# Kernel tuning notes

Measured on AMD Instinct MI355X. Metric: run time of the kernel, lower is better.

Reference implementation:

```python
import jax, jax.numpy as jnp
import numpy as np

N, M, D = 2048, 100000, 128
K = 5


def setup_inputs() -> dict:
    key = jax.random.key(0)
    k1, k2 = jax.random.split(key)
    features = jax.random.normal(k1, (N, D), dtype=jnp.float32)
    memory_bank = jax.random.normal(k2, (M, D), dtype=jnp.float32)
    # normalization buffers computed during fit(); use plausible scalars
    min_val = jnp.zeros((), dtype=jnp.float32)
    max_val = jnp.ones((), dtype=jnp.float32)
    return {
        "features": features,
        "memory_bank": memory_bank,
        "min_val": min_val,
        "max_val": max_val,
        "n_neighbors": K,
    }


def reference(features, memory_bank, min_val, max_val, n_neighbors):
    x2 = jnp.sum(features * features, axis=1, keepdims=True)        # (N,1)
    y2 = jnp.sum(memory_bank * memory_bank, axis=1)[None, :]        # (1,M)
    d2 = x2 + y2 - 2.0 * (features @ memory_bank.T)                 # (N,M)
    dist = jnp.sqrt(jnp.maximum(d2, 0.0))
    # k smallest distances per query (topk largest=False)
    neg_knn, _ = jax.lax.top_k(-dist, n_neighbors)                  # (N,K)
    knn = -neg_knn
    # min-max normalization with fitted stats
    knn = (knn - min_val) / (max_val - min_val)
    return knn.mean(axis=1)                                         # (N,)
```

## Files before the change

### kernel.cpp

```cpp
#include <hip/hip_runtime.h>
#include <stdint.h>

#define N_Q 2048
#define M_B 100000
#define D_DIM 128
#define KNN 5
#define SLABS_TOTAL 1563
#define M_PAD (SLABS_TOTAL * 64)
#define CHUNKS 64
#define SPC 25
#define CLS 16
#define FTOT (CHUNKS * CLS)
#define ROWBLOCKS 8
#define TROWS 256
#define RT 4
#define BIGF 3.0e38f
#define NEGF -3.0e38f


typedef __attribute__((ext_vector_type(8))) short short8;
typedef __attribute__((ext_vector_type(4))) unsigned short ushort4v;
typedef __attribute__((ext_vector_type(8))) unsigned short ushort8v;
typedef __attribute__((ext_vector_type(4))) float f32x4;

static __device__ __forceinline__ unsigned short f2bf(float f) {
  unsigned int u = __builtin_bit_cast(unsigned int, f);
  u = (u + 0x7FFFu + ((u >> 16) & 1u)) >> 16;
  return (unsigned short)u;
}

static __device__ __forceinline__ void gload_lds16(const void* g, void* l) {
  __builtin_amdgcn_global_load_lds((const __attribute__((address_space(1))) unsigned int*)g,
                                   (__attribute__((address_space(3))) unsigned int*)l, 16, 0, 0);
}
static __device__ __forceinline__ void gload_lds4(const void* g, void* l) {
  __builtin_amdgcn_global_load_lds((const __attribute__((address_space(1))) unsigned int*)g,
                                   (__attribute__((address_space(3))) unsigned int*)l, 4, 0, 0);
}

#define DPPADD(v, ctrl)                                                              \
  do {                                                                               \
    int _t = __builtin_amdgcn_update_dpp(0, __builtin_bit_cast(int, (v)), (ctrl),    \
                                         0xf, 0xf, false);                           \
    (v) = (v) + __builtin_bit_cast(float, _t);                                       \
  } while (0)

__global__ __launch_bounds__(256) void k_prep(const float* __restrict__ Y,
                                              unsigned short* __restrict__ ybf,
                                              float* __restrict__ ny2) {
  const int s = blockIdx.x;
  const int t = threadIdx.x;
  __shared__ __align__(16) unsigned short tile[8192];
  __shared__ float redy[64 * 33];
#pragma unroll
  for (int i = 0; i < 8; ++i) {
    const int u = i * 256 + t;
    const int rowl = u >> 5;
    const int q = u & 31;
    const int rowg = s * 64 + rowl;
    const int rowc = (rowg < M_B) ? rowg : (M_B - 1);
    const float4 v = ((const float4*)Y)[(size_t)rowc * 32 + q];
    redy[rowl * 33 + q] = v.x * v.x + v.y * v.y + v.z * v.z + v.w * v.w;
    ushort4v o;
    o[0] = f2bf(v.x); o[1] = f2bf(v.y); o[2] = f2bf(v.z); o[3] = f2bf(v.w);
    *(ushort4v*)(tile + (size_t)(((q >> 1) * 64 + rowl) * 8 + (q & 1) * 4)) = o;
  }
  __syncthreads();
  {
    const int rowl = t >> 2;
    const int k = t & 3;
    float ss = 0.f;
#pragma unroll
    for (int j = 0; j < 8; ++j) ss += redy[rowl * 33 + k * 8 + j];
    DPPADD(ss, 0xB1);
    DPPADD(ss, 0x4E);
    const int rowg = s * 64 + rowl;
    if ((t & 3) == 0) ny2[(size_t)s * 64 + rowl] = (rowg < M_B) ? (-0.5f * ss) : NEGF;
  }
#pragma unroll
  for (int i = 0; i < 4; ++i) {
    const int u = i * 256 + t;
    *(ushort8v*)(ybf + ((size_t)s * 1024 + u) * 8) = *(const ushort8v*)(tile + u * 8);
  }
}

__global__ __launch_bounds__(256, 2) void k_main(const float* __restrict__ X,
                                                 const unsigned short* __restrict__ ybf,
                                                 const float* __restrict__ ny2,
                                                 float* __restrict__ rsm) {
  __shared__ __align__(16) char smem[39168];
  unsigned short* ys = (unsigned short*)smem;
  float* ny2s = (float*)(smem + 32768);

  const int bid = blockIdx.x;
  const int chunk = bid % CHUNKS;
  const int rowblock = bid / CHUNKS;
  const int row0 = rowblock * TROWS;

  const int cs0 = chunk * SPC;
  int nslab = SLABS_TOTAL - cs0;
  if (nslab > SPC) nslab = SPC;
  if (nslab < 0) nslab = 0;

  const int t = threadIdx.x;
  const int wave = t >> 6;
  const int lane = t & 63;
  const int lm = lane & 15;
  const int lq = lane >> 4;

  short8 afrag[RT][4];
#pragma unroll
  for (int rt = 0; rt < RT; ++rt)
#pragma unroll
    for (int ks = 0; ks < 4; ++ks) {
      const float* xr = X + (size_t)(row0 + wave * 64 + rt * 16 + lm) * D_DIM + ks * 32 + lq * 8;
      const float4 a = *(const float4*)xr;
      const float4 b = *(const float4*)(xr + 4);
      short8 f;
      f[0] = (short)f2bf(a.x); f[1] = (short)f2bf(a.y);
      f[2] = (short)f2bf(a.z); f[3] = (short)f2bf(a.w);
      f[4] = (short)f2bf(b.x); f[5] = (short)f2bf(b.y);
      f[6] = (short)f2bf(b.z); f[7] = (short)f2bf(b.w);
      afrag[rt][ks] = f;
    }

  for (int j = wave; j < nslab; j += 4)
    gload_lds4(ny2 + (size_t)(cs0 + j) * 64 + lane, ny2s + (size_t)j * 64);
  __syncthreads();

  float prmax[RT][4];
#pragma unroll
  for (int rt = 0; rt < RT; ++rt)
#pragma unroll
    for (int rr = 0; rr < 4; ++rr) prmax[rt][rr] = NEGF;

  if (nslab > 0) {
    const unsigned short* src = ybf + (size_t)cs0 * 8192;
#pragma unroll
    for (int i = 0; i < 4; ++i) {
      const int ub = i * 256 + wave * 64;
      gload_lds16(src + (size_t)(ub + lane) * 8, ys + (size_t)ub * 8);
    }
  }

  for (int s = 0; s < nslab; ++s) {
    unsigned short* yb = ys + (size_t)(s & 1) * 8192;
    if (s + 1 < nslab) {
      const unsigned short* src = ybf + (size_t)(cs0 + s + 1) * 8192;
      unsigned short* dst = ys + (size_t)((s + 1) & 1) * 8192;
#pragma unroll
      for (int i = 0; i < 4; ++i) {
        const int ub = i * 256 + wave * 64;
        gload_lds16(src + (size_t)(ub + lane) * 8, dst + (size_t)ub * 8);
      }
      asm volatile("s_waitcnt vmcnt(4)" ::: "memory");
    } else {
      asm volatile("s_waitcnt vmcnt(0)" ::: "memory");
    }
    __builtin_amdgcn_s_barrier();

    float y2c[4];
#pragma unroll
    for (int ct = 0; ct < 4; ++ct) y2c[ct] = ny2s[s * 64 + ct * 16 + lm];

    f32x4 acc[RT][4];
#pragma unroll
    for (int rt = 0; rt < RT; ++rt)
#pragma unroll
      for (int ct = 0; ct < 4; ++ct)
#pragma unroll
        for (int rr = 0; rr < 4; ++rr) acc[rt][ct][rr] = y2c[ct];

    __builtin_amdgcn_s_setprio(1);
#pragma unroll
    for (int ct = 0; ct < 4; ++ct) {
      short8 bfr[4];
#pragma unroll
      for (int ks = 0; ks < 4; ++ks)
        bfr[ks] = *(const short8*)(yb + (size_t)(((ks * 4 + lq) * 64 + ct * 16 + lm)) * 8);
#pragma unroll
      for (int rt = 0; rt < RT; ++rt)
#pragma unroll
        for (int ks = 0; ks < 4; ++ks)
          acc[rt][ct] = __builtin_amdgcn_mfma_f32_16x16x32_bf16(afrag[rt][ks], bfr[ks],
                                                                acc[rt][ct], 0, 0, 0);
    }
    __builtin_amdgcn_s_setprio(0);

#pragma unroll
    for (int rt = 0; rt < RT; ++rt)
#pragma unroll
      for (int rr = 0; rr < 4; ++rr) {
        const float cm = fmaxf(fmaxf(fmaxf(acc[rt][0][rr], acc[rt][1][rr]),
                                     acc[rt][2][rr]), acc[rt][3][rr]);
        prmax[rt][rr] = fmaxf(prmax[rt][rr], cm);
      }

    __builtin_amdgcn_s_barrier();
  }

#pragma unroll
  for (int rt = 0; rt < RT; ++rt)
#pragma unroll
    for (int rr = 0; rr < 4; ++rr) {
      const int lrow = wave * 64 + rt * 16 + lq * 4 + rr;
      rsm[(size_t)(row0 + lrow) * FTOT + chunk * CLS + lm] = prmax[rt][rr];
    }
}

__global__ __launch_bounds__(256) void k_scan(const float* __restrict__ rsm,
                                              const float* __restrict__ X,
                                              const float* __restrict__ minp,
                                              const float* __restrict__ maxp,
                                              float* __restrict__ out) {
  const int wave = threadIdx.x >> 6;
  const int lane = threadIdx.x & 63;
  const int row = blockIdx.x * 4 + wave;
  const float* rp = rsm + (size_t)row * FTOT;

  float x2;
  {
    const float a = X[(size_t)row * D_DIM + lane];
    const float b = X[(size_t)row * D_DIM + 64 + lane];
    x2 = a * a + b * b;
#pragma unroll
    for (int off = 1; off < 64; off <<= 1) x2 += __shfl_xor(x2, off);
  }

  float t0 = NEGF, t1 = NEGF, t2 = NEGF, t3 = NEGF, t4 = NEGF;
  for (int i = lane; i < FTOT; i += 64) {
    const float v = rp[i];
    if (v > t4) {
      float m = v;
      float n3 = fminf(t3, m); m = fmaxf(t3, m);
      float n2 = fminf(t2, m); m = fmaxf(t2, m);
      float n1 = fminf(t1, m); m = fmaxf(t1, m);
      float n0 = fminf(t0, m); m = fmaxf(t0, m);
      t0 = m; t1 = n0; t2 = n1; t3 = n2; t4 = n3;
    }
  }

  int k = 0;
  float sum = 0.f;
#pragma unroll
  for (int r = 0; r < KNN; ++r) {
    float head = (k == 0) ? t0 : (k == 1) ? t1 : (k == 2) ? t2 : (k == 3) ? t3
               : (k == 4) ? t4 : NEGF;
    float m = head;
#pragma unroll
    for (int off = 1; off < 64; off <<= 1) m = fmaxf(m, __shfl_xor(m, off));
    const unsigned long long mask = __ballot(head == m);
    const int first = __ffsll(mask) - 1;
    if (lane == first) ++k;
    sum += sqrtf(fmaxf(x2 - 2.f * m, 0.f));
  }
  if (lane == 0) {
    const float mn = minp[0], mx = maxp[0];
    out[row] = (sum * (1.0f / KNN) - mn) / (mx - mn);
  }
}

extern "C" void kernel_launch(void* const* d_in, const int* in_sizes, int n_in,
                              void* d_out, int out_size, void* d_ws, size_t ws_size,
                              hipStream_t stream) {
  const float* X = (const float*)d_in[0];
  const float* Y = (const float*)d_in[1];
  const float* minp = (const float*)d_in[2];
  const float* maxp = (const float*)d_in[3];
  float* out = (float*)d_out;

  char* ws = (char*)d_ws;
  size_t off = 0;
  unsigned short* ybf = (unsigned short*)(ws + off); off += (size_t)M_PAD * D_DIM * 2;
  float* ny2 = (float*)(ws + off);                   off += (size_t)M_PAD * 4;
  float* rsm = (float*)(ws + off);                   off += (size_t)N_Q * FTOT * 4;

  k_prep<<<dim3(SLABS_TOTAL), dim3(256), 0, stream>>>(Y, ybf, ny2);
  k_main<<<dim3(ROWBLOCKS * CHUNKS), dim3(256), 0, stream>>>(X, ybf, ny2, rsm);
  k_scan<<<dim3(N_Q / 4), dim3(256), 0, stream>>>(rsm, X, minp, maxp, out);
}
```

Before: 149.7 us.

## Split memory bank into more chunks and cut accumulator registers for 3 blocks/CU

Raises the number of memory-bank chunks from 64 to 96 (17 slabs each), which gives more blocks and a larger per-row partial-max buffer for the scan kernel. The MFMA accumulation now runs one column tile at a time, so only 4 accumulators are live instead of 16. Together with a smaller LDS buffer, this is meant to allow 3 blocks per CU. The ks loop is moved outside the rt loop to interleave independent MFMAs, and the priority hints are dropped. In exchange, the max reduction runs per column tile, and the scan kernel reads more partials per row.

```diff
diff --git a/kernel.cpp b/kernel.cpp
--- a/kernel.cpp
+++ b/kernel.cpp
@@ -7,13 +7,12 @@
 #define KNN 5
 #define SLABS_TOTAL 1563
 #define M_PAD (SLABS_TOTAL * 64)
-#define CHUNKS 64
-#define SPC 25
+#define CHUNKS 96
+#define SPC 17
 #define CLS 16
 #define FTOT (CHUNKS * CLS)
 #define ROWBLOCKS 8
 #define TROWS 256
-#define RT 4
 #define BIGF 3.0e38f
 #define NEGF -3.0e38f
 
@@ -84,11 +83,11 @@
   }
 }
 
-__global__ __launch_bounds__(256, 2) void k_main(const float* __restrict__ X,
+__global__ __launch_bounds__(256, 3) void k_main(const float* __restrict__ X,
                                                  const unsigned short* __restrict__ ybf,
                                                  const float* __restrict__ ny2,
                                                  float* __restrict__ rsm) {
-  __shared__ __align__(16) char smem[39168];
+  __shared__ __align__(16) char smem[37120];
   unsigned short* ys = (unsigned short*)smem;
   float* ny2s = (float*)(smem + 32768);
 
@@ -108,9 +107,9 @@
   const int lm = lane & 15;
   const int lq = lane >> 4;
 
-  short8 afrag[RT][4];
-#pragma unroll
-  for (int rt = 0; rt < RT; ++rt)
+  short8 afrag[4][4];
+#pragma unroll
+  for (int rt = 0; rt < 4; ++rt)
 #pragma unroll
     for (int ks = 0; ks < 4; ++ks) {
       const float* xr = X + (size_t)(row0 + wave * 64 + rt * 16 + lm) * D_DIM + ks * 32 + lq * 8;
@@ -128,9 +127,9 @@
     gload_lds4(ny2 + (size_t)(cs0 + j) * 64 + lane, ny2s + (size_t)j * 64);
   __syncthreads();
 
-  float prmax[RT][4];
-#pragma unroll
-  for (int rt = 0; rt < RT; ++rt)
+  float prmax[4][4];
+#pragma unroll
+  for (int rt = 0; rt < 4; ++rt)
 #pragma unroll
     for (int rr = 0; rr < 4; ++rr) prmax[rt][rr] = NEGF;
 
@@ -144,10 +143,10 @@
   }
 
   for (int s = 0; s < nslab; ++s) {
-    unsigned short* yb = ys + (size_t)(s & 1) * 8192;
+    const unsigned short* yb = ys + (size_t)((s & 1) * 8192);
     if (s + 1 < nslab) {
       const unsigned short* src = ybf + (size_t)(cs0 + s + 1) * 8192;
-      unsigned short* dst = ys + (size_t)((s + 1) & 1) * 8192;
+      unsigned short* dst = ys + (size_t)(((s + 1) & 1) * 8192);
 #pragma unroll
       for (int i = 0; i < 4; ++i) {
         const int ub = i * 256 + wave * 64;
@@ -159,48 +158,40 @@
     }
     __builtin_amdgcn_s_barrier();
 
-    float y2c[4];
-#pragma unroll
-    for (int ct = 0; ct < 4; ++ct) y2c[ct] = ny2s[s * 64 + ct * 16 + lm];
-
-    f32x4 acc[RT][4];
-#pragma unroll
-    for (int rt = 0; rt < RT; ++rt)
-#pragma unroll
-      for (int ct = 0; ct < 4; ++ct)
-#pragma unroll
-        for (int rr = 0; rr < 4; ++rr) acc[rt][ct][rr] = y2c[ct];
-
-    __builtin_amdgcn_s_setprio(1);
 #pragma unroll
     for (int ct = 0; ct < 4; ++ct) {
+      const float yc = ny2s[s * 64 + ct * 16 + lm];
+
       short8 bfr[4];
 #pragma unroll
       for (int ks = 0; ks < 4; ++ks)
         bfr[ks] = *(const short8*)(yb + (size_t)(((ks * 4 + lq) * 64 + ct * 16 + lm)) * 8);
-#pragma unroll
-      for (int rt = 0; rt < RT; ++rt)
-#pragma unroll
-        for (int ks = 0; ks < 4; ++ks)
-          acc[rt][ct] = __builtin_amdgcn_mfma_f32_16x16x32_bf16(afrag[rt][ks], bfr[ks],
-                                                                acc[rt][ct], 0, 0, 0);
-    }
-    __builtin_amdgcn_s_setprio(0);
-
-#pragma unroll
-    for (int rt = 0; rt < RT; ++rt)
-#pragma unroll
-      for (int rr = 0; rr < 4; ++rr) {
-        const float cm = fmaxf(fmaxf(fmaxf(acc[rt][0][rr], acc[rt][1][rr]),
-                                     acc[rt][2][rr]), acc[rt][3][rr]);
-        prmax[rt][rr] = fmaxf(prmax[rt][rr], cm);
-      }
+
+      f32x4 acc[4];
+#pragma unroll
+      for (int rt = 0; rt < 4; ++rt)
+#pragma unroll
+        for (int rr = 0; rr < 4; ++rr) acc[rt][rr] = yc;
+
+#pragma unroll
+      for (int ks = 0; ks < 4; ++ks)
+#pragma unroll
+        for (int rt = 0; rt < 4; ++rt)
+          acc[rt] = __builtin_amdgcn_mfma_f32_16x16x32_bf16(afrag[rt][ks], bfr[ks],
+                                                            acc[rt], 0, 0, 0);
+
+#pragma unroll
+      for (int rt = 0; rt < 4; ++rt)
+#pragma unroll
+        for (int rr = 0; rr < 4; ++rr)
+          prmax[rt][rr] = fmaxf(prmax[rt][rr], acc[rt][rr]);
+    }
 
     __builtin_amdgcn_s_barrier();
   }
 
 #pragma unroll
-  for (int rt = 0; rt < RT; ++rt)
+  for (int rt = 0; rt < 4; ++rt)
 #pragma unroll
     for (int rr = 0; rr < 4; ++rr) {
       const int lrow = wave * 64 + rt * 16 + lq * 4 + rr;
```

Measured after the change: 150.1 us. No clear change (+0.3%).
